# Performance work log

Measured on AMD Instinct MI355X. Metric: run time of the kernel, lower is better.

The kernel has to match this reference:

```python
import jax, jax.numpy as jnp
import numpy as np

H = 8192  # hidden_dimension
D = 8192  # trailing feature width of x


def setup_inputs() -> dict:
    key = jax.random.key(0)
    k_x, k_w = jax.random.split(key)
    x = jax.random.normal(k_x, (H, D), dtype=jnp.float32)
    # torch.nn.init.uniform_(weights, 0, 0.9); bias initialized to 0
    weights = jax.random.uniform(k_w, (H - 1, 1), dtype=jnp.float32, minval=0.0, maxval=0.9)
    bias = jnp.zeros((H - 1, 1), dtype=jnp.float32)
    return {"x": x, "weights": weights, "bias": bias}


def reference(x, weights, bias):
    # Original: for 5 generations, y[i] = x[i] + x[i-1]*w[i-1] + b[i-1] (i>0),
    # reading from the ORIGINAL x each time -> idempotent, single affine op.
    # weights/bias are [H-1, 1] and broadcast over the trailing D axis.
    shifted = x[1:] + x[:-1] * weights + bias  # [H-1, D]
    y = jnp.concatenate([x[:1], shifted], axis=0)  # [H, D]
    return y
```

## Files before the change

kernel.cpp:

```cpp
#include <hip/hip_runtime.h>


#define H_DIM 8192
#define D_DIM 8192
#define D4 (D_DIM / 4)
#define ROWS_PER_CHUNK 32
#define BLOCK 256

__global__ __launch_bounds__(BLOCK) void lateral_kernel(
    const float4* __restrict__ x,
    const float* __restrict__ w,
    const float* __restrict__ b,
    float4* __restrict__ y) {

    const int col = blockIdx.x * BLOCK + threadIdx.x;
    const int r0  = blockIdx.y * ROWS_PER_CHUNK;

    float4 prev;
    int rstart;
    if (r0 == 0) {
        float4 cur = x[col];
        y[col] = cur;
        prev = cur;
        rstart = 1;
    } else {
        prev = x[(size_t)(r0 - 1) * D4 + col];
        rstart = r0;
    }

    const int rend = r0 + ROWS_PER_CHUNK;
    #pragma unroll 4
    for (int i = rstart; i < rend; ++i) {
        float4 cur = x[(size_t)i * D4 + col];
        float wi = w[i - 1];
        float bi = b[i - 1];
        float4 o;
        o.x = fmaf(prev.x, wi, cur.x + bi);
        o.y = fmaf(prev.y, wi, cur.y + bi);
        o.z = fmaf(prev.z, wi, cur.z + bi);
        o.w = fmaf(prev.w, wi, cur.w + bi);
        y[(size_t)i * D4 + col] = o;
        prev = cur;
    }
}

extern "C" void kernel_launch(void* const* d_in, const int* in_sizes, int n_in,
                              void* d_out, int out_size, void* d_ws, size_t ws_size,
                              hipStream_t stream) {
    const float4* x = (const float4*)d_in[0];
    const float*  w = (const float*)d_in[1];
    const float*  b = (const float*)d_in[2];
    float4* y = (float4*)d_out;

    dim3 grid(D4 / BLOCK, H_DIM / ROWS_PER_CHUNK);
    dim3 block(BLOCK);
    lateral_kernel<<<grid, block, 0, stream>>>(x, w, b, y);
}
```

Baseline: 444.1 us.

## Flatten to one float4 per thread with nontemporal stores

Replaces the per-column, 32-row chunk loop that carried the previous row in a register with a flat 1D grid where each thread handles one float4. Each thread loads both its own element and the element one row above, and writes the result with a nontemporal store. This aims for more memory-level parallelism and less cache pollution from output writes. In exchange, each x element is read twice, relying on the L2/MALL cache to absorb the second read.

```diff
diff --git a/kernel.cpp b/kernel.cpp
--- a/kernel.cpp
+++ b/kernel.cpp
@@ -4,55 +4,43 @@
 #define H_DIM 8192
 #define D_DIM 8192
 #define D4 (D_DIM / 4)
-#define ROWS_PER_CHUNK 32
+#define N4 (H_DIM * D4)
 #define BLOCK 256
 
-__global__ __launch_bounds__(BLOCK) void lateral_kernel(
-    const float4* __restrict__ x,
+typedef float v4f __attribute__((ext_vector_type(4)));
+
+__global__ __launch_bounds__(BLOCK, 8) void lateral_kernel(
+    const v4f* __restrict__ x,
     const float* __restrict__ w,
     const float* __restrict__ b,
-    float4* __restrict__ y) {
+    v4f* __restrict__ y) {
 
-    const int col = blockIdx.x * BLOCK + threadIdx.x;
-    const int r0  = blockIdx.y * ROWS_PER_CHUNK;
+    const int idx = blockIdx.x * BLOCK + threadIdx.x;
 
-    float4 prev;
-    int rstart;
-    if (r0 == 0) {
-        float4 cur = x[col];
-        y[col] = cur;
-        prev = cur;
-        rstart = 1;
+    v4f cur = x[idx];
+    v4f o;
+    if (idx >= D4) {
+        const int row = idx >> 11;
+        v4f pv = x[idx - D4];
+        const float wi = w[row - 1];
+        const float bi = b[row - 1];
+        o.x = fmaf(pv.x, wi, cur.x + bi);
+        o.y = fmaf(pv.y, wi, cur.y + bi);
+        o.z = fmaf(pv.z, wi, cur.z + bi);
+        o.w = fmaf(pv.w, wi, cur.w + bi);
     } else {
-        prev = x[(size_t)(r0 - 1) * D4 + col];
-        rstart = r0;
+        o = cur;
     }
-
-    const int rend = r0 + ROWS_PER_CHUNK;
-    #pragma unroll 4
-    for (int i = rstart; i < rend; ++i) {
-        float4 cur = x[(size_t)i * D4 + col];
-        float wi = w[i - 1];
-        float bi = b[i - 1];
-        float4 o;
-        o.x = fmaf(prev.x, wi, cur.x + bi);
-        o.y = fmaf(prev.y, wi, cur.y + bi);
-        o.z = fmaf(prev.z, wi, cur.z + bi);
-        o.w = fmaf(prev.w, wi, cur.w + bi);
-        y[(size_t)i * D4 + col] = o;
-        prev = cur;
-    }
+    __builtin_nontemporal_store(o, &y[idx]);
 }
 
 extern "C" void kernel_launch(void* const* d_in, const int* in_sizes, int n_in,
                               void* d_out, int out_size, void* d_ws, size_t ws_size,
                               hipStream_t stream) {
-    const float4* x = (const float4*)d_in[0];
-    const float*  w = (const float*)d_in[1];
-    const float*  b = (const float*)d_in[2];
-    float4* y = (float4*)d_out;
+    const v4f*   x = (const v4f*)d_in[0];
+    const float* w = (const float*)d_in[1];
+    const float* b = (const float*)d_in[2];
+    v4f* y = (v4f*)d_out;
 
-    dim3 grid(D4 / BLOCK, H_DIM / ROWS_PER_CHUNK);
-    dim3 block(BLOCK);
-    lateral_kernel<<<grid, block, 0, stream>>>(x, w, b, y);
+    lateral_kernel<<<N4 / BLOCK, BLOCK, 0, stream>>>(x, w, b, y);
 }
```

After: 425.3 us. 4.2% less time.
